# Optimization experiments

Hardware: AMD Instinct MI355X
Metric: run time of the kernel (lower is better)

The kernel has to match this reference:

```python
import jax, jax.numpy as jnp
import numpy as np

EMB = 768
HEADS = 8

def setup_inputs() -> dict:
    key = jax.random.key(0)
    ks = jax.random.split(key, 9)
    B, N, E = 16, 1024, EMB
    s = 1.0 / np.sqrt(E)
    x = jax.random.normal(ks[0], (B, N, E), dtype=jnp.float32)
    Wq = jax.random.normal(ks[1], (E, E), dtype=jnp.float32) * s
    bq = jnp.zeros((E,), dtype=jnp.float32)
    Wk = jax.random.normal(ks[2], (E, E), dtype=jnp.float32) * s
    bk = jnp.zeros((E,), dtype=jnp.float32)
    Wv = jax.random.normal(ks[3], (E, E), dtype=jnp.float32) * s
    bv = jnp.zeros((E,), dtype=jnp.float32)
    Wo = jax.random.normal(ks[4], (E, E), dtype=jnp.float32) * s
    bo = jnp.zeros((E,), dtype=jnp.float32)
    return {"x": x, "Wq": Wq, "bq": bq, "Wk": Wk, "bk": bk, "Wv": Wv, "bv": bv, "Wo": Wo, "bo": bo}

def reference(x, Wq, bq, Wk, bk, Wv, bv, Wo, bo):
    B, N, E = x.shape
    H = HEADS
    D = E // H
    # separate Q/K/V linears, split heads: b n (h d) -> b h n d
    q = (x @ Wq + bq).reshape(B, N, H, D).transpose(0, 2, 1, 3)
    k = (x @ Wk + bk).reshape(B, N, H, D).transpose(0, 2, 1, 3)
    v = (x @ Wv + bv).reshape(B, N, H, D).transpose(0, 2, 1, 3)
    energy = jnp.einsum('bhqd,bhkd->bhqk', q, k)
    # NON-STANDARD: softmax first, then divide by sqrt(emb_size)
    scaling = jnp.float32(E) ** 0.5
    attn = jax.nn.softmax(energy, axis=-1) / scaling
    out = jnp.einsum('bhqk,bhkd->bhqd', attn, v)
    out = out.transpose(0, 2, 1, 3).reshape(B, N, E)  # b h n d -> b n (h d)
    return out @ Wo + bo
```

## Files before the change

kernel.cpp:

```cpp
#include <hip/hip_runtime.h>


typedef _Float16 half8 __attribute__((ext_vector_type(8)));
typedef float f32x4 __attribute__((ext_vector_type(4)));

__device__ __forceinline__ void gload_lds16(const void* g, void* l) {
  __builtin_amdgcn_global_load_lds((const __attribute__((address_space(1))) void*)g,
                                   (__attribute__((address_space(3))) void*)l, 16, 0, 0);
}


__global__ __launch_bounds__(256) void conv_x_kernel(const float* __restrict__ x,
                                                     _Float16* __restrict__ xh) {
  long i = ((long)blockIdx.x * 256 + threadIdx.x) * 8;
  float4 a = *(const float4*)(x + i);
  float4 b = *(const float4*)(x + i + 4);
  half8 o;
  o[0] = (_Float16)a.x; o[1] = (_Float16)a.y; o[2] = (_Float16)a.z; o[3] = (_Float16)a.w;
  o[4] = (_Float16)b.x; o[5] = (_Float16)b.y; o[6] = (_Float16)b.z; o[7] = (_Float16)b.w;
  *(half8*)(xh + i) = o;
}

__global__ __launch_bounds__(256) void transpose_cvt_kernel(
    const float* __restrict__ W0, const float* __restrict__ W1,
    const float* __restrict__ W2, const float* __restrict__ W3,
    _Float16* __restrict__ WT) {
  __shared__ float tile[32][33];
  int z = blockIdx.z;
  const float* W = (z == 0) ? W0 : (z == 1) ? W1 : (z == 2) ? W2 : W3;
  int k0 = blockIdx.y * 32, n0 = blockIdx.x * 32;
  int tx = threadIdx.x, ty = threadIdx.y;
#pragma unroll
  for (int j = ty; j < 32; j += 8)
    tile[j][tx] = W[(size_t)(k0 + j) * 768 + n0 + tx];
  __syncthreads();
  _Float16* dst = WT + (size_t)z * 768 * 768;
#pragma unroll
  for (int j = ty; j < 32; j += 8)
    dst[(size_t)(n0 + j) * 768 + k0 + tx] = (_Float16)tile[tx][j];
}

__global__ __launch_bounds__(256) void conv_bias_kernel(const float* __restrict__ bq,
                                                        const float* __restrict__ bk,
                                                        const float* __restrict__ bv,
                                                        float* __restrict__ bias) {
  int i = blockIdx.x * 256 + threadIdx.x;
  if (i >= 2304) return;
  bias[i] = (i < 768) ? bq[i] : (i < 1536) ? bk[i - 768] : bv[i - 1536];
}


template <int OUT_F16>
__global__ __launch_bounds__(256) void gemm_nt_kernel(
    const _Float16* __restrict__ A, const _Float16* __restrict__ Bt,
    const float* __restrict__ bias, void* __restrict__ C,
    int M, int N, int K, int ldc) {
  __shared__ _Float16 As[128 * 32];
  __shared__ _Float16 Bs[128 * 32];
  int nbx = N >> 7;
  int nwg = gridDim.x;
  int wg = blockIdx.x;
  int cpx = nwg >> 3;
  int swz = (wg & 7) * cpx + (wg >> 3);
  int bx = swz % nbx, by = swz / nbx;
  int m0 = by * 128, n0 = bx * 128;
  int t = threadIdx.x, l = t & 63, w = t >> 6;
  int lg = l >> 4, lr = l & 15;
  int wr = w >> 1, wc = w & 1;
  f32x4 acc[4][4] = {};

  for (int k0 = 0; k0 < K; k0 += 32) {
    __syncthreads();
#pragma unroll
    for (int j = 0; j < 2; ++j) {
      int slot = j * 256 + t;
      gload_lds16(A + (size_t)(m0 + (slot >> 2)) * K + k0 + (slot & 3) * 8, &As[slot * 8]);
    }
#pragma unroll
    for (int j = 0; j < 2; ++j) {
      int slot = j * 256 + t;
      gload_lds16(Bt + (size_t)(n0 + (slot >> 2)) * K + k0 + (slot & 3) * 8, &Bs[slot * 8]);
    }
    __syncthreads();
    half8 af[4], bf[4];
#pragma unroll
    for (int r = 0; r < 4; ++r) af[r] = *(const half8*)&As[(wr * 64 + r * 16 + lr) * 32 + lg * 8];
#pragma unroll
    for (int c = 0; c < 4; ++c) bf[c] = *(const half8*)&Bs[(wc * 64 + c * 16 + lr) * 32 + lg * 8];
#pragma unroll
    for (int r = 0; r < 4; ++r)
#pragma unroll
      for (int c = 0; c < 4; ++c)
        acc[r][c] = __builtin_amdgcn_mfma_f32_16x16x32_f16(af[r], bf[c], acc[r][c], 0, 0, 0);
  }

#pragma unroll
  for (int r = 0; r < 4; ++r)
#pragma unroll
    for (int c = 0; c < 4; ++c) {
      int col = n0 + wc * 64 + c * 16 + lr;
      float bb = bias[col];
#pragma unroll
      for (int i = 0; i < 4; ++i) {
        int row = m0 + wr * 64 + r * 16 + lg * 4 + i;
        float v = acc[r][c][i] + bb;
        if (OUT_F16)
          ((_Float16*)C)[(size_t)row * ldc + col] = (_Float16)v;
        else
          ((float*)C)[(size_t)row * ldc + col] = v;
      }
    }
}


__global__ __launch_bounds__(512) void attn_kernel(const _Float16* __restrict__ QKV,
                                                   _Float16* __restrict__ Oh) {
  constexpr float LOG2E = 1.4426950408889634f;
  int hw = blockIdx.x;
  int lin = (hw & 7) * 128 + (hw >> 3);
  int bh = lin >> 3, qt = lin & 7;
  int b = bh >> 3, h = bh & 7;
  int t = threadIdx.x, w = t >> 6, l = t & 63;
  int lg = l >> 4, lr = l & 15;

  __shared__ _Float16 Ks[2][64 * 128];
  __shared__ _Float16 Vts[2][96 * 64];
  __shared__ _Float16 Ps[8][16 * 64];

  const _Float16* Qb = QKV + (size_t)b * 1024 * 2304 + h * 96;
  const _Float16* Kb = Qb + 768;
  const _Float16* Vb = Qb + 1536;

  half8 qf[3];
  {
    int qrow = qt * 128 + w * 16 + lr;
#pragma unroll
    for (int c = 0; c < 3; ++c)
      qf[c] = *(const half8*)&Qb[(size_t)qrow * 2304 + c * 32 + lg * 8];
  }

  auto stage = [&](int kv0, int bi) {
#pragma unroll
    for (int j = 0; j < 2; ++j) {
      int slot = j * 512 + t;
      int kv = slot >> 4, seg = slot & 15;
      int segr = seg ^ (kv & 7);
      gload_lds16(Kb + (size_t)(kv0 + kv) * 2304 + segr * 8, &Ks[bi][slot * 8]);
    }
    if (t < 384) {
      int kvp = t / 12, m = t % 12;
      half8 v0 = *(const half8*)&Vb[(size_t)(kv0 + 2 * kvp) * 2304 + m * 8];
      half8 v1 = *(const half8*)&Vb[(size_t)(kv0 + 2 * kvp + 1) * 2304 + m * 8];
#pragma unroll
      for (int e = 0; e < 8; ++e) {
        int d = m * 8 + e;
        int sw = ((d & 7) ^ ((d >> 3) & 7)) << 3;
        union { _Float16 h2[2]; unsigned u32; } pk;
        pk.h2[0] = v0[e]; pk.h2[1] = v1[e];
        *(unsigned*)&Vts[bi][d * 64 + ((2 * kvp) ^ sw)] = pk.u32;
      }
    }
  };

  float m_run = -3.0e38f, l_run = 0.f;
  f32x4 o_acc[6] = {};

  stage(0, 0);

  for (int tile = 0; tile < 16; ++tile) {
    int bi = tile & 1;
    __syncthreads();
    if (tile + 1 < 16) stage((tile + 1) * 64, bi ^ 1);

    f32x4 s_acc[4];
#pragma unroll
    for (int tt = 0; tt < 4; ++tt) {
      s_acc[tt] = f32x4{0.f, 0.f, 0.f, 0.f};
      int kvr = tt * 16 + lr;
#pragma unroll
      for (int c = 0; c < 3; ++c) {
        half8 kf = *(const half8*)&Ks[bi][kvr * 128 + ((c * 4 + lg) ^ (kvr & 7)) * 8];
        s_acc[tt] = __builtin_amdgcn_mfma_f32_16x16x32_f16(kf, qf[c], s_acc[tt], 0, 0, 0);
      }
    }

    float tmax = -3.0e38f;
#pragma unroll
    for (int tt = 0; tt < 4; ++tt)
#pragma unroll
      for (int i = 0; i < 4; ++i) tmax = fmaxf(tmax, s_acc[tt][i]);
    tmax = fmaxf(tmax, __shfl_xor(tmax, 16, 64));
    tmax = fmaxf(tmax, __shfl_xor(tmax, 32, 64));
    float m_new = fmaxf(m_run, tmax);
    float scale = __builtin_exp2f((m_run - m_new) * LOG2E);
    float rs = 0.f;
    _Float16 ph[4][4];
#pragma unroll
    for (int tt = 0; tt < 4; ++tt)
#pragma unroll
      for (int i = 0; i < 4; ++i) {
        float p = __builtin_exp2f((s_acc[tt][i] - m_new) * LOG2E);
        rs += p;
        ph[tt][i] = (_Float16)p;
      }
    rs += __shfl_xor(rs, 16, 64);
    rs += __shfl_xor(rs, 32, 64);
    l_run = l_run * scale + rs;
    m_run = m_new;

    {
      int swq = (lr & 7) << 3;
#pragma unroll
      for (int tt = 0; tt < 4; ++tt)
#pragma unroll
        for (int ip = 0; ip < 2; ++ip) {
          int kvb = tt * 16 + lg * 4 + ip * 2;
          union { _Float16 h2[2]; unsigned u32; } pk;
          pk.h2[0] = ph[tt][ip * 2]; pk.h2[1] = ph[tt][ip * 2 + 1];
          *(unsigned*)&Ps[w][lr * 64 + (kvb ^ swq)] = pk.u32;
        }
    }

    float sc0 = __shfl(scale, lg * 4 + 0, 64);
    float sc1 = __shfl(scale, lg * 4 + 1, 64);
    float sc2 = __shfl(scale, lg * 4 + 2, 64);
    float sc3 = __shfl(scale, lg * 4 + 3, 64);
#pragma unroll
    for (int cc = 0; cc < 6; ++cc) {
      o_acc[cc][0] *= sc0; o_acc[cc][1] *= sc1;
      o_acc[cc][2] *= sc2; o_acc[cc][3] *= sc3;
    }

#pragma unroll
    for (int kc = 0; kc < 2; ++kc) {
      half8 pf = *(const half8*)&Ps[w][lr * 64 + ((kc * 32 + lg * 8) ^ ((lr & 7) << 3))];
#pragma unroll
      for (int cc = 0; cc < 6; ++cc) {
        int d = cc * 16 + lr;
        int sw = ((d & 7) ^ ((d >> 3) & 7)) << 3;
        half8 vf = *(const half8*)&Vts[bi][d * 64 + ((kc * 32 + lg * 8) ^ sw)];
        o_acc[cc] = __builtin_amdgcn_mfma_f32_16x16x32_f16(pf, vf, o_acc[cc], 0, 0, 0);
      }
    }
  }

  float inv = 1.0f / (l_run * 27.712812921102035f);
  float iv0 = __shfl(inv, lg * 4 + 0, 64);
  float iv1 = __shfl(inv, lg * 4 + 1, 64);
  float iv2 = __shfl(inv, lg * 4 + 2, 64);
  float iv3 = __shfl(inv, lg * 4 + 3, 64);
  size_t rbase = (size_t)(b * 1024 + qt * 128 + w * 16) * 768 + h * 96;
#pragma unroll
  for (int cc = 0; cc < 6; ++cc) {
    int col = cc * 16 + lr;
    Oh[rbase + (size_t)(lg * 4 + 0) * 768 + col] = (_Float16)(o_acc[cc][0] * iv0);
    Oh[rbase + (size_t)(lg * 4 + 1) * 768 + col] = (_Float16)(o_acc[cc][1] * iv1);
    Oh[rbase + (size_t)(lg * 4 + 2) * 768 + col] = (_Float16)(o_acc[cc][2] * iv2);
    Oh[rbase + (size_t)(lg * 4 + 3) * 768 + col] = (_Float16)(o_acc[cc][3] * iv3);
  }
}


extern "C" void kernel_launch(void* const* d_in, const int* in_sizes, int n_in,
                              void* d_out, int out_size, void* d_ws, size_t ws_size,
                              hipStream_t stream) {
  const float* x  = (const float*)d_in[0];
  const float* Wq = (const float*)d_in[1];
  const float* bq = (const float*)d_in[2];
  const float* Wk = (const float*)d_in[3];
  const float* bk = (const float*)d_in[4];
  const float* Wv = (const float*)d_in[5];
  const float* bv = (const float*)d_in[6];
  const float* Wo = (const float*)d_in[7];
  const float* bo = (const float*)d_in[8];
  float* out = (float*)d_out;

  char* ws = (char*)d_ws;
  _Float16* WT   = (_Float16*)(ws);
  float*    bias = (float*)(ws + 4718592);
  _Float16* xh   = (_Float16*)(ws + 4751360);
  _Float16* QKV  = (_Float16*)(ws + 29917184);
  _Float16* Oh   = (_Float16*)(ws + 105414656);

  conv_x_kernel<<<6144, 256, 0, stream>>>(x, xh);
  transpose_cvt_kernel<<<dim3(24, 24, 4), dim3(32, 8), 0, stream>>>(Wq, Wk, Wv, Wo, WT);
  conv_bias_kernel<<<9, 256, 0, stream>>>(bq, bk, bv, bias);

  gemm_nt_kernel<1><<<2304, 256, 0, stream>>>(xh, WT, bias, QKV, 16384, 2304, 768, 2304);

  attn_kernel<<<1024, 512, 0, stream>>>(QKV, Oh);

  gemm_nt_kernel<0><<<768, 256, 0, stream>>>(Oh, WT + (size_t)2304 * 768, bo, out,
                                             16384, 768, 768, 768);
}
```

Measured before the change: 240.7 us.

## Fold log2e into Q, skip lazy rescale, pack P stores, hoist staging offsets

Pre-multiplies Q by log2(e) in fp16 so the softmax exponentials no longer need a per-element multiply. Rescaling of the output accumulator and running sum is skipped unless the running max grows by more than a threshold. P values are converted with packed round-toward-zero and written as 64-bit stores, and the K/V staging addresses are computed once outside the loop. Together these cut VALU and LDS instruction count in the attention inner loop, in exchange for small accuracy changes from the fp16 Q scaling, rtz rounding and exponents allowed to exceed 1 by up to 2^11.5.

```diff
diff --git a/kernel.cpp b/kernel.cpp
--- a/kernel.cpp
+++ b/kernel.cpp
@@ -2,6 +2,7 @@
 
 
 typedef _Float16 half8 __attribute__((ext_vector_type(8)));
+typedef __fp16 fp16x2 __attribute__((ext_vector_type(2)));
 typedef float f32x4 __attribute__((ext_vector_type(4)));
 
 __device__ __forceinline__ void gload_lds16(const void* g, void* l) {
@@ -115,7 +116,6 @@
 
 __global__ __launch_bounds__(512) void attn_kernel(const _Float16* __restrict__ QKV,
                                                    _Float16* __restrict__ Oh) {
-  constexpr float LOG2E = 1.4426950408889634f;
   int hw = blockIdx.x;
   int lin = (hw & 7) * 128 + (hw >> 3);
   int bh = lin >> 3, qt = lin & 7;
@@ -134,30 +134,52 @@
   half8 qf[3];
   {
     int qrow = qt * 128 + w * 16 + lr;
-#pragma unroll
-    for (int c = 0; c < 3; ++c)
+    const _Float16 s = (_Float16)1.4426950408889634f;
+#pragma unroll
+    for (int c = 0; c < 3; ++c) {
       qf[c] = *(const half8*)&Qb[(size_t)qrow * 2304 + c * 32 + lg * 8];
-  }
+#pragma unroll
+      for (int e = 0; e < 8; ++e) qf[c][e] = qf[c][e] * s;
+    }
+  }
+
+  int ksrc[2], kdst[2];
+#pragma unroll
+  for (int j = 0; j < 2; ++j) {
+    int slot = j * 512 + t;
+    int kv = slot >> 4, seg = slot & 15;
+    ksrc[j] = kv * 2304 + (seg ^ (kv & 7)) * 8;
+    kdst[j] = slot * 8;
+  }
+  bool vact = t < 384;
+  int kvp = t / 12, m = t % 12;
+  int vsrc = 2 * kvp * 2304 + m * 8;
+  int vdst[8];
+#pragma unroll
+  for (int e = 0; e < 8; ++e) {
+    int d = m * 8 + e;
+    int sw = ((d & 7) ^ ((d >> 3) & 7)) << 3;
+    vdst[e] = d * 64 + ((2 * kvp) ^ sw);
+  }
+  int swq = (lr & 7) << 3;
+  int poff[4];
+#pragma unroll
+  for (int tt = 0; tt < 4; ++tt) poff[tt] = lr * 64 + ((tt * 16 + lg * 4) ^ swq);
 
   auto stage = [&](int kv0, int bi) {
-#pragma unroll
-    for (int j = 0; j < 2; ++j) {
-      int slot = j * 512 + t;
-      int kv = slot >> 4, seg = slot & 15;
-      int segr = seg ^ (kv & 7);
-      gload_lds16(Kb + (size_t)(kv0 + kv) * 2304 + segr * 8, &Ks[bi][slot * 8]);
-    }
-    if (t < 384) {
-      int kvp = t / 12, m = t % 12;
-      half8 v0 = *(const half8*)&Vb[(size_t)(kv0 + 2 * kvp) * 2304 + m * 8];
-      half8 v1 = *(const half8*)&Vb[(size_t)(kv0 + 2 * kvp + 1) * 2304 + m * 8];
+    size_t goff = (size_t)kv0 * 2304;
+#pragma unroll
+    for (int j = 0; j < 2; ++j)
+      gload_lds16(Kb + goff + ksrc[j], &Ks[bi][kdst[j]]);
+    if (vact) {
+      const _Float16* vp = Vb + goff + vsrc;
+      half8 v0 = *(const half8*)vp;
+      half8 v1 = *(const half8*)(vp + 2304);
 #pragma unroll
       for (int e = 0; e < 8; ++e) {
-        int d = m * 8 + e;
-        int sw = ((d & 7) ^ ((d >> 3) & 7)) << 3;
         union { _Float16 h2[2]; unsigned u32; } pk;
         pk.h2[0] = v0[e]; pk.h2[1] = v1[e];
-        *(unsigned*)&Vts[bi][d * 64 + ((2 * kvp) ^ sw)] = pk.u32;
+        *(unsigned*)&Vts[bi][vdst[e]] = pk.u32;
       }
     }
   };
@@ -191,49 +213,43 @@
       for (int i = 0; i < 4; ++i) tmax = fmaxf(tmax, s_acc[tt][i]);
     tmax = fmaxf(tmax, __shfl_xor(tmax, 16, 64));
     tmax = fmaxf(tmax, __shfl_xor(tmax, 32, 64));
-    float m_new = fmaxf(m_run, tmax);
-    float scale = __builtin_exp2f((m_run - m_new) * LOG2E);
+
+    if (!__all(tmax <= m_run + 11.5f)) {
+      float m_new = fmaxf(m_run, tmax);
+      float scale = __builtin_exp2f(m_run - m_new);
+      float sc0 = __shfl(scale, lg * 4 + 0, 64);
+      float sc1 = __shfl(scale, lg * 4 + 1, 64);
+      float sc2 = __shfl(scale, lg * 4 + 2, 64);
+      float sc3 = __shfl(scale, lg * 4 + 3, 64);
+#pragma unroll
+      for (int cc = 0; cc < 6; ++cc) {
+        o_acc[cc][0] *= sc0; o_acc[cc][1] *= sc1;
+        o_acc[cc][2] *= sc2; o_acc[cc][3] *= sc3;
+      }
+      l_run *= scale;
+      m_run = m_new;
+    }
+
     float rs = 0.f;
-    _Float16 ph[4][4];
-#pragma unroll
-    for (int tt = 0; tt < 4; ++tt)
-#pragma unroll
-      for (int i = 0; i < 4; ++i) {
-        float p = __builtin_exp2f((s_acc[tt][i] - m_new) * LOG2E);
-        rs += p;
-        ph[tt][i] = (_Float16)p;
-      }
+#pragma unroll
+    for (int tt = 0; tt < 4; ++tt) {
+      float p0 = __builtin_exp2f(s_acc[tt][0] - m_run);
+      float p1 = __builtin_exp2f(s_acc[tt][1] - m_run);
+      float p2 = __builtin_exp2f(s_acc[tt][2] - m_run);
+      float p3 = __builtin_exp2f(s_acc[tt][3] - m_run);
+      rs += (p0 + p1) + (p2 + p3);
+      union { fp16x2 h2[2]; unsigned long long u64; } pk;
+      pk.h2[0] = __builtin_amdgcn_cvt_pkrtz(p0, p1);
+      pk.h2[1] = __builtin_amdgcn_cvt_pkrtz(p2, p3);
+      *(unsigned long long*)&Ps[w][poff[tt]] = pk.u64;
+    }
     rs += __shfl_xor(rs, 16, 64);
     rs += __shfl_xor(rs, 32, 64);
-    l_run = l_run * scale + rs;
-    m_run = m_new;
-
-    {
-      int swq = (lr & 7) << 3;
-#pragma unroll
-      for (int tt = 0; tt < 4; ++tt)
-#pragma unroll
-        for (int ip = 0; ip < 2; ++ip) {
-          int kvb = tt * 16 + lg * 4 + ip * 2;
-          union { _Float16 h2[2]; unsigned u32; } pk;
-          pk.h2[0] = ph[tt][ip * 2]; pk.h2[1] = ph[tt][ip * 2 + 1];
-          *(unsigned*)&Ps[w][lr * 64 + (kvb ^ swq)] = pk.u32;
-        }
-    }
-
-    float sc0 = __shfl(scale, lg * 4 + 0, 64);
-    float sc1 = __shfl(scale, lg * 4 + 1, 64);
-    float sc2 = __shfl(scale, lg * 4 + 2, 64);
-    float sc3 = __shfl(scale, lg * 4 + 3, 64);
-#pragma unroll
-    for (int cc = 0; cc < 6; ++cc) {
-      o_acc[cc][0] *= sc0; o_acc[cc][1] *= sc1;
-      o_acc[cc][2] *= sc2; o_acc[cc][3] *= sc3;
-    }
+    l_run += rs;
 
 #pragma unroll
     for (int kc = 0; kc < 2; ++kc) {
-      half8 pf = *(const half8*)&Ps[w][lr * 64 + ((kc * 32 + lg * 8) ^ ((lr & 7) << 3))];
+      half8 pf = *(const half8*)&Ps[w][lr * 64 + ((kc * 32 + lg * 8) ^ swq)];
 #pragma unroll
       for (int cc = 0; cc < 6; ++cc) {
         int d = cc * 16 + lr;
```

Result: faster. 231.8 us (-3.7%).
